# Kernel optimization log

Hardware: AMD Instinct MI355X
Metric: run time of the kernel (lower is better)

Reference implementation:

```python
import jax, jax.numpy as jnp
import numpy as np

N_QUBITS = 4
N_LAYERS = 2
MARGIN = 0.3
BATCH = 524288
DIM = 2 ** N_QUBITS  # 16


def _apply_ry(state, theta, q):
    # state: [B, 16] complex; theta: [B] real; RY on qubit q (qubit 0 = MSB)
    B = state.shape[0]
    lead = 2 ** q
    rest = 2 ** (N_QUBITS - q - 1)
    s = state.reshape(B, lead, 2, rest)
    c = jnp.cos(theta * 0.5)[:, None, None]
    sn = jnp.sin(theta * 0.5)[:, None, None]
    a0, a1 = s[:, :, 0, :], s[:, :, 1, :]
    out = jnp.stack([c * a0 - sn * a1, sn * a0 + c * a1], axis=2)
    return out.reshape(B, DIM)


def _apply_rz(state, theta, q):
    B = state.shape[0]
    lead = 2 ** q
    rest = 2 ** (N_QUBITS - q - 1)
    s = state.reshape(B, lead, 2, rest)
    ph = jnp.exp(1j * (theta * 0.5)).astype(jnp.complex64)[:, None, None]
    a0, a1 = s[:, :, 0, :], s[:, :, 1, :]
    out = jnp.stack([jnp.conj(ph) * a0, ph * a1], axis=2)
    return out.reshape(B, DIM)


def _apply_cnot(state, c, t):
    # c < t; control qubit c, target qubit t
    B = state.shape[0]
    s = state.reshape((B,) + (2,) * N_QUBITS)
    s0 = jnp.take(s, 0, axis=c + 1)
    s1 = jnp.take(s, 1, axis=c + 1)
    s1 = jnp.flip(s1, axis=t)  # t > c: target axis shifts to t after removing axis c+1
    out = jnp.stack([s0, s1], axis=c + 1)
    return out.reshape(B, DIM)


def _simulate(ry, rz):
    # ry, rz: [B, N_LAYERS, N_QUBITS] -> statevector [B, 16] complex64
    B = ry.shape[0]
    state = jnp.zeros((B, DIM), dtype=jnp.complex64).at[:, 0].set(1.0)
    for l in range(N_LAYERS):
        for q in range(N_QUBITS):
            state = _apply_ry(state, ry[:, l, q], q)
            state = _apply_rz(state, rz[:, l, q], q)
        for q in range(N_QUBITS - 1):  # linear entangling chain
            state = _apply_cnot(state, q, q + 1)
    return state


def setup_inputs() -> dict:
    key = jax.random.key(0)
    ks = jax.random.split(key, 6)
    shape = (BATCH, N_LAYERS, N_QUBITS)
    names = ["anchor_ry", "anchor_rz", "positive_ry", "positive_rz",
             "negative_ry", "negative_rz"]
    return {n: jax.random.normal(k, shape, dtype=jnp.float32)
            for n, k in zip(names, ks)}


def reference(anchor_ry, anchor_rz, positive_ry, positive_rz,
              negative_ry, negative_rz):
    psi_a = _simulate(anchor_ry, anchor_rz)
    psi_p = _simulate(positive_ry, positive_rz)
    psi_n = _simulate(negative_ry, negative_rz)
    # fidelity |<a|b>|^2 per sample
    ov_p = jnp.sum(jnp.conj(psi_a) * psi_p, axis=-1)
    ov_n = jnp.sum(jnp.conj(psi_a) * psi_n, axis=-1)
    fid_pos = jnp.abs(ov_p) ** 2
    fid_neg = jnp.abs(ov_n) ** 2
    loss = jnp.maximum(MARGIN - fid_pos + fid_neg, 0.0)
    return loss.mean()
```

## Files before the change

### kernel.cpp

```cpp
#include <hip/hip_runtime.h>

typedef float v2f __attribute__((ext_vector_type(2)));

constexpr int NQ = 4;
constexpr int DIM = 16;
constexpr float MARGIN = 0.3f;
constexpr float INV2PI = 0.15915494309189535f;

__device__ __forceinline__ v2f mk2(float x, float y) { v2f r; r.x = x; r.y = y; return r; }

__device__ __forceinline__ v2f cmul_pre(v2f a, v2f b, v2f bs) {
  return a.xx * b + a.yy * bs;
}

__device__ __forceinline__ void sincos_hw(float rev, float& s, float& c) {
  s = __builtin_amdgcn_sinf(rev);
  c = __builtin_amdgcn_cosf(rev);
}

__device__ __forceinline__ void cnot_ladder(v2f s[DIM]) {
#pragma unroll
  for (int q = 0; q < NQ - 1; ++q) {
    const int pc = 1 << (NQ - 1 - q);
    const int pt = 1 << (NQ - 2 - q);
#pragma unroll
    for (int i = 0; i < DIM; ++i) {
      if ((i & pc) && !(i & pt)) {
        const int j = i | pt;
        v2f t = s[i]; s[i] = s[j]; s[j] = t;
      }
    }
  }
}

__device__ __forceinline__ void simulate(const float ry[8], const float rz[8], v2f s[DIM]) {
  float c0[NQ]; v2f p1[NQ], p1s[NQ];
#pragma unroll
  for (int q = 0; q < NQ; ++q) {
    float sy, cy; sincos_hw(ry[q] * (0.5f * INV2PI), sy, cy);
    float sz, cz; sincos_hw(rz[q] * INV2PI, sz, cz);
    c0[q]  = cy;
    p1[q]  = mk2(sy * cz, sy * sz);
    p1s[q] = mk2(-p1[q].y, p1[q].x);
  }
  v2f t2[4];
  t2[0] = mk2(c0[0] * c0[1], 0.0f);
  t2[1] = c0[0] * p1[1];
  t2[2] = c0[1] * p1[0];
  t2[3] = cmul_pre(p1[0], p1[1], p1s[1]);
  v2f t3[8];
#pragma unroll
  for (int k = 0; k < 4; ++k) {
    t3[2*k]   = t2[k] * c0[2];
    t3[2*k+1] = cmul_pre(t2[k], p1[2], p1s[2]);
  }
#pragma unroll
  for (int k = 0; k < 8; ++k) {
    s[2*k]   = t3[k] * c0[3];
    s[2*k+1] = cmul_pre(t3[k], p1[3], p1s[3]);
  }

  cnot_ladder(s);

#pragma unroll
  for (int q = 0; q < NQ; ++q) {
    const int bit = 1 << (NQ - 1 - q);
    float sy, cy; sincos_hw(ry[4 + q] * (0.5f * INV2PI), sy, cy);
#pragma unroll
    for (int i = 0; i < DIM; ++i) {
      if (i & bit) continue;
      const int j = i | bit;
      const v2f a0 = s[i], a1 = s[j];
      s[i] = cy * a0 - sy * a1;
      s[j] = sy * a0 + cy * a1;
    }
    float sz, cz; sincos_hw(rz[4 + q] * INV2PI, sz, cz);
    const v2f ph  = mk2(cz, sz);
    const v2f phs = mk2(-sz, cz);
#pragma unroll
    for (int i = 0; i < DIM; ++i) {
      if (i & bit) s[i] = cmul_pre(s[i], ph, phs);
    }
  }
}

__device__ __forceinline__ float fidelity(const v2f a[DIM], const v2f x[DIM]) {
  v2f ov1 = mk2(0.f, 0.f), ov2 = mk2(0.f, 0.f);
#pragma unroll
  for (int i = 0; i < DIM; ++i) {
    ov1 += a[i].xx * x[i];
    ov2 += a[i].yy * x[i].yx;
  }
  const float ovr = ov1.x + ov2.x;
  const float ovi = ov1.y - ov2.y;
  return ovr * ovr + ovi * ovi;
}

__device__ __forceinline__ void load8(const float* __restrict__ p, int b, float a[8]) {
  const float4* v = reinterpret_cast<const float4*>(p) + (size_t)b * 2;
  float4 x0 = v[0], x1 = v[1];
  a[0]=x0.x; a[1]=x0.y; a[2]=x0.z; a[3]=x0.w;
  a[4]=x1.x; a[5]=x1.y; a[6]=x1.z; a[7]=x1.w;
}

__global__ __launch_bounds__(256) void triplet_main(
    const float* __restrict__ a_ry, const float* __restrict__ a_rz,
    const float* __restrict__ p_ry, const float* __restrict__ p_rz,
    const float* __restrict__ n_ry, const float* __restrict__ n_rz,
    float* __restrict__ block_sums, int batch) {
  const int b = blockIdx.x * blockDim.x + threadIdx.x;

  float loss = 0.0f;
  if (b < batch) {
    float ry[8], rz[8];
    load8(a_ry, b, ry); load8(a_rz, b, rz);
    v2f as[DIM];
    simulate(ry, rz, as);

    load8(p_ry, b, ry); load8(p_rz, b, rz);
    v2f xs[DIM];
    simulate(ry, rz, xs);
    const float fid_pos = fidelity(as, xs);

    load8(n_ry, b, ry); load8(n_rz, b, rz);
    simulate(ry, rz, xs);
    const float fid_neg = fidelity(as, xs);

    loss = fmaxf(MARGIN - fid_pos + fid_neg, 0.0f);
  }

#pragma unroll
  for (int off = 32; off >= 1; off >>= 1)
    loss += __shfl_down(loss, off, 64);

  __shared__ float wsum[4];
  const int lane = threadIdx.x & 63;
  const int wid  = threadIdx.x >> 6;
  if (lane == 0) wsum[wid] = loss;
  __syncthreads();
  if (threadIdx.x == 0) {
    block_sums[blockIdx.x] = wsum[0] + wsum[1] + wsum[2] + wsum[3];
  }
}

__global__ __launch_bounds__(256) void triplet_reduce(
    const float* __restrict__ block_sums, int nblocks, float* __restrict__ out, float inv_batch) {
  float s = 0.0f;
  for (int i = threadIdx.x; i < nblocks; i += 256) s += block_sums[i];
#pragma unroll
  for (int off = 32; off >= 1; off >>= 1)
    s += __shfl_down(s, off, 64);

  __shared__ float wsum[4];
  const int lane = threadIdx.x & 63;
  const int wid  = threadIdx.x >> 6;
  if (lane == 0) wsum[wid] = s;
  __syncthreads();
  if (threadIdx.x == 0) {
    out[0] = (wsum[0] + wsum[1] + wsum[2] + wsum[3]) * inv_batch;
  }
}

extern "C" void kernel_launch(void* const* d_in, const int* in_sizes, int n_in,
                              void* d_out, int out_size, void* d_ws, size_t ws_size,
                              hipStream_t stream) {
  const float* a_ry = (const float*)d_in[0];
  const float* a_rz = (const float*)d_in[1];
  const float* p_ry = (const float*)d_in[2];
  const float* p_rz = (const float*)d_in[3];
  const float* n_ry = (const float*)d_in[4];
  const float* n_rz = (const float*)d_in[5];
  float* out = (float*)d_out;

  const int batch = in_sizes[0] / 8;
  const int nblocks = (batch + 255) / 256;
  float* block_sums = (float*)d_ws;

  triplet_main<<<nblocks, 256, 0, stream>>>(a_ry, a_rz, p_ry, p_rz, n_ry, n_rz,
                                            block_sums, batch);
  triplet_reduce<<<1, 256, 0, stream>>>(block_sums, nblocks, out, 1.0f / (float)batch);
}
```

Baseline: 29.46 us.

## Fold anchor's final RZ phases into other states and fuse reduction via last-block atomic

Drops the last-layer RZ from the anchor state and applies only the phase differences (rz_p - rz_a, rz_n - rz_a) to the positive and negative states. This works because the overlap's magnitude is unchanged by the common diagonal phase. It also interleaves the positive and negative simulations for ILP and loads all inputs up front. The separate reduce kernel is replaced by a last-block-done atomic counter, at the cost of a memset launch and threadfences.

```diff
diff --git a/kernel.cpp b/kernel.cpp
--- a/kernel.cpp
+++ b/kernel.cpp
@@ -33,7 +33,7 @@
   }
 }
 
-__device__ __forceinline__ void simulate(const float ry[8], const float rz[8], v2f s[DIM]) {
+__device__ __forceinline__ void layer1_cl(const float ry[8], const float rz[8], v2f s[DIM]) {
   float c0[NQ]; v2f p1[NQ], p1s[NQ];
 #pragma unroll
   for (int q = 0; q < NQ; ++q) {
@@ -59,9 +59,10 @@
     s[2*k]   = t3[k] * c0[3];
     s[2*k+1] = cmul_pre(t3[k], p1[3], p1s[3]);
   }
-
   cnot_ladder(s);
-
+}
+
+__device__ __forceinline__ void ry_layer(const float ry[8], v2f s[DIM]) {
 #pragma unroll
   for (int q = 0; q < NQ; ++q) {
     const int bit = 1 << (NQ - 1 - q);
@@ -74,26 +75,7 @@
       s[i] = cy * a0 - sy * a1;
       s[j] = sy * a0 + cy * a1;
     }
-    float sz, cz; sincos_hw(rz[4 + q] * INV2PI, sz, cz);
-    const v2f ph  = mk2(cz, sz);
-    const v2f phs = mk2(-sz, cz);
-#pragma unroll
-    for (int i = 0; i < DIM; ++i) {
-      if (i & bit) s[i] = cmul_pre(s[i], ph, phs);
-    }
-  }
-}
-
-__device__ __forceinline__ float fidelity(const v2f a[DIM], const v2f x[DIM]) {
-  v2f ov1 = mk2(0.f, 0.f), ov2 = mk2(0.f, 0.f);
-#pragma unroll
-  for (int i = 0; i < DIM; ++i) {
-    ov1 += a[i].xx * x[i];
-    ov2 += a[i].yy * x[i].yx;
-  }
-  const float ovr = ov1.x + ov2.x;
-  const float ovi = ov1.y - ov2.y;
-  return ovr * ovr + ovi * ovi;
+  }
 }
 
 __device__ __forceinline__ void load8(const float* __restrict__ p, int b, float a[8]) {
@@ -103,28 +85,77 @@
   a[4]=x1.x; a[5]=x1.y; a[6]=x1.z; a[7]=x1.w;
 }
 
-__global__ __launch_bounds__(256) void triplet_main(
+__global__ __launch_bounds__(256) void triplet_fused(
     const float* __restrict__ a_ry, const float* __restrict__ a_rz,
     const float* __restrict__ p_ry, const float* __restrict__ p_rz,
     const float* __restrict__ n_ry, const float* __restrict__ n_rz,
-    float* __restrict__ block_sums, int batch) {
+    float* __restrict__ partials, unsigned* __restrict__ counter,
+    float* __restrict__ out, int batch) {
   const int b = blockIdx.x * blockDim.x + threadIdx.x;
 
   float loss = 0.0f;
   if (b < batch) {
-    float ry[8], rz[8];
-    load8(a_ry, b, ry); load8(a_rz, b, rz);
+    float ary[8], arz[8];
+    load8(a_ry, b, ary); load8(a_rz, b, arz);
     v2f as[DIM];
-    simulate(ry, rz, as);
-
-    load8(p_ry, b, ry); load8(p_rz, b, rz);
-    v2f xs[DIM];
-    simulate(ry, rz, xs);
-    const float fid_pos = fidelity(as, xs);
-
-    load8(n_ry, b, ry); load8(n_rz, b, rz);
-    simulate(ry, rz, xs);
-    const float fid_neg = fidelity(as, xs);
+    layer1_cl(ary, arz, as);
+    ry_layer(ary, as);
+
+    float pry[8], prz[8], nry[8], nrz[8];
+    load8(p_ry, b, pry); load8(p_rz, b, prz);
+    load8(n_ry, b, nry); load8(n_rz, b, nrz);
+
+    v2f xs[DIM], ys[DIM];
+    layer1_cl(pry, prz, xs);
+    layer1_cl(nry, nrz, ys);
+
+#pragma unroll
+    for (int q = 0; q < NQ; ++q) {
+      const int bit = 1 << (NQ - 1 - q);
+      float syp, cyp; sincos_hw(pry[4 + q] * (0.5f * INV2PI), syp, cyp);
+      float syn, cyn; sincos_hw(nry[4 + q] * (0.5f * INV2PI), syn, cyn);
+#pragma unroll
+      for (int i = 0; i < DIM; ++i) {
+        if (i & bit) continue;
+        const int j = i | bit;
+        const v2f x0 = xs[i], x1 = xs[j];
+        xs[i] = cyp * x0 - syp * x1;
+        xs[j] = syp * x0 + cyp * x1;
+        const v2f y0 = ys[i], y1 = ys[j];
+        ys[i] = cyn * y0 - syn * y1;
+        ys[j] = syn * y0 + cyn * y1;
+      }
+    }
+
+#pragma unroll
+    for (int q = 0; q < NQ; ++q) {
+      const int bit = 1 << (NQ - 1 - q);
+      float szp, czp; sincos_hw((prz[4 + q] - arz[4 + q]) * INV2PI, szp, czp);
+      float szn, czn; sincos_hw((nrz[4 + q] - arz[4 + q]) * INV2PI, szn, czn);
+      const v2f php  = mk2(czp, szp), phps = mk2(-szp, czp);
+      const v2f phn  = mk2(czn, szn), phns = mk2(-szn, czn);
+#pragma unroll
+      for (int i = 0; i < DIM; ++i) {
+        if (i & bit) {
+          xs[i] = cmul_pre(xs[i], php, phps);
+          ys[i] = cmul_pre(ys[i], phn, phns);
+        }
+      }
+    }
+
+    v2f op1 = mk2(0.f,0.f), op2 = mk2(0.f,0.f);
+    v2f on1 = mk2(0.f,0.f), on2 = mk2(0.f,0.f);
+#pragma unroll
+    for (int i = 0; i < DIM; ++i) {
+      op1 += as[i].xx * xs[i];
+      op2 += as[i].yy * xs[i].yx;
+      on1 += as[i].xx * ys[i];
+      on2 += as[i].yy * ys[i].yx;
+    }
+    const float opr = op1.x + op2.x, opi = op1.y - op2.y;
+    const float onr = on1.x + on2.x, oni = on1.y - on2.y;
+    const float fid_pos = opr*opr + opi*opi;
+    const float fid_neg = onr*onr + oni*oni;
 
     loss = fmaxf(MARGIN - fid_pos + fid_neg, 0.0f);
   }
@@ -138,26 +169,27 @@
   const int wid  = threadIdx.x >> 6;
   if (lane == 0) wsum[wid] = loss;
   __syncthreads();
+
+  __shared__ bool amLast;
   if (threadIdx.x == 0) {
-    block_sums[blockIdx.x] = wsum[0] + wsum[1] + wsum[2] + wsum[3];
-  }
-}
-
-__global__ __launch_bounds__(256) void triplet_reduce(
-    const float* __restrict__ block_sums, int nblocks, float* __restrict__ out, float inv_batch) {
-  float s = 0.0f;
-  for (int i = threadIdx.x; i < nblocks; i += 256) s += block_sums[i];
-#pragma unroll
-  for (int off = 32; off >= 1; off >>= 1)
-    s += __shfl_down(s, off, 64);
-
-  __shared__ float wsum[4];
-  const int lane = threadIdx.x & 63;
-  const int wid  = threadIdx.x >> 6;
-  if (lane == 0) wsum[wid] = s;
+    partials[blockIdx.x] = wsum[0] + wsum[1] + wsum[2] + wsum[3];
+    __threadfence();
+    unsigned old = atomicAdd(counter, 1u);
+    amLast = (old == gridDim.x - 1);
+  }
   __syncthreads();
-  if (threadIdx.x == 0) {
-    out[0] = (wsum[0] + wsum[1] + wsum[2] + wsum[3]) * inv_batch;
+
+  if (amLast) {
+    __threadfence();
+    float s = 0.0f;
+    for (int i = threadIdx.x; i < (int)gridDim.x; i += 256) s += partials[i];
+#pragma unroll
+    for (int off = 32; off >= 1; off >>= 1)
+      s += __shfl_down(s, off, 64);
+    if (lane == 0) wsum[wid] = s;
+    __syncthreads();
+    if (threadIdx.x == 0)
+      out[0] = (wsum[0] + wsum[1] + wsum[2] + wsum[3]) / (float)batch;
   }
 }
 
@@ -174,9 +206,12 @@
 
   const int batch = in_sizes[0] / 8;
   const int nblocks = (batch + 255) / 256;
-  float* block_sums = (float*)d_ws;
-
-  triplet_main<<<nblocks, 256, 0, stream>>>(a_ry, a_rz, p_ry, p_rz, n_ry, n_rz,
-                                            block_sums, batch);
-  triplet_reduce<<<1, 256, 0, stream>>>(block_sums, nblocks, out, 1.0f / (float)batch);
-}
+
+  float* partials = (float*)d_ws;
+  unsigned* counter = (unsigned*)((char*)d_ws + (size_t)nblocks * sizeof(float));
+
+  hipMemsetAsync(counter, 0, sizeof(unsigned), stream);
+
+  triplet_fused<<<nblocks, 256, 0, stream>>>(a_ry, a_rz, p_ry, p_rz, n_ry, n_rz,
+                                             partials, counter, out, batch);
+}
```

New measurement: 86.91 us. 2.95x slower.

## Fold final RZ layer into relative phase and fuse reduction via last-block atomic

Applied to the files above, without the earlier changes.

The last-layer RZ gates are diagonal, so the overlap only depends on the difference of the final RZ angles. Instead of applying them to every state, only the positive and negative states get a phase of the angle difference, which drops the anchor's final RZ sincos and multiplies. The separate reduce kernel is replaced by a last-block-done pattern: an atomic counter plus threadfence, with the final block summing the partials. This adds a memset launch and an atomic per block, and sets launch_bounds min blocks to 1.

```diff
diff --git a/kernel.cpp b/kernel.cpp
--- a/kernel.cpp
+++ b/kernel.cpp
@@ -33,7 +33,7 @@
   }
 }
 
-__device__ __forceinline__ void simulate(const float ry[8], const float rz[8], v2f s[DIM]) {
+__device__ __forceinline__ void sim_core(const float ry[8], const float rz[8], v2f s[DIM]) {
   float c0[NQ]; v2f p1[NQ], p1s[NQ];
 #pragma unroll
   for (int q = 0; q < NQ; ++q) {
@@ -74,17 +74,21 @@
       s[i] = cy * a0 - sy * a1;
       s[j] = sy * a0 + cy * a1;
     }
-    float sz, cz; sincos_hw(rz[4 + q] * INV2PI, sz, cz);
+  }
+}
+
+__device__ __forceinline__ float fid_with_dz(const v2f a[DIM], v2f x[DIM], const float dz[NQ]) {
+#pragma unroll
+  for (int q = 0; q < NQ; ++q) {
+    const int bit = 1 << (NQ - 1 - q);
+    float sz, cz; sincos_hw(dz[q] * INV2PI, sz, cz);
     const v2f ph  = mk2(cz, sz);
     const v2f phs = mk2(-sz, cz);
 #pragma unroll
     for (int i = 0; i < DIM; ++i) {
-      if (i & bit) s[i] = cmul_pre(s[i], ph, phs);
+      if (i & bit) x[i] = cmul_pre(x[i], ph, phs);
     }
   }
-}
-
-__device__ __forceinline__ float fidelity(const v2f a[DIM], const v2f x[DIM]) {
   v2f ov1 = mk2(0.f, 0.f), ov2 = mk2(0.f, 0.f);
 #pragma unroll
   for (int i = 0; i < DIM; ++i) {
@@ -103,28 +107,37 @@
   a[4]=x1.x; a[5]=x1.y; a[6]=x1.z; a[7]=x1.w;
 }
 
-__global__ __launch_bounds__(256) void triplet_main(
+__global__ __launch_bounds__(256, 1) void triplet_fused(
     const float* __restrict__ a_ry, const float* __restrict__ a_rz,
     const float* __restrict__ p_ry, const float* __restrict__ p_rz,
     const float* __restrict__ n_ry, const float* __restrict__ n_rz,
-    float* __restrict__ block_sums, int batch) {
+    float* __restrict__ partials, unsigned* __restrict__ counter,
+    float* __restrict__ out, int batch) {
   const int b = blockIdx.x * blockDim.x + threadIdx.x;
 
   float loss = 0.0f;
   if (b < batch) {
-    float ry[8], rz[8];
+    float ry[8], rz[8], arz2[NQ];
+
     load8(a_ry, b, ry); load8(a_rz, b, rz);
+#pragma unroll
+    for (int q = 0; q < NQ; ++q) arz2[q] = rz[4 + q];
     v2f as[DIM];
-    simulate(ry, rz, as);
+    sim_core(ry, rz, as);
 
     load8(p_ry, b, ry); load8(p_rz, b, rz);
     v2f xs[DIM];
-    simulate(ry, rz, xs);
-    const float fid_pos = fidelity(as, xs);
+    sim_core(ry, rz, xs);
+    float dz[NQ];
+#pragma unroll
+    for (int q = 0; q < NQ; ++q) dz[q] = rz[4 + q] - arz2[q];
+    const float fid_pos = fid_with_dz(as, xs, dz);
 
     load8(n_ry, b, ry); load8(n_rz, b, rz);
-    simulate(ry, rz, xs);
-    const float fid_neg = fidelity(as, xs);
+    sim_core(ry, rz, xs);
+#pragma unroll
+    for (int q = 0; q < NQ; ++q) dz[q] = rz[4 + q] - arz2[q];
+    const float fid_neg = fid_with_dz(as, xs, dz);
 
     loss = fmaxf(MARGIN - fid_pos + fid_neg, 0.0f);
   }
@@ -138,26 +151,27 @@
   const int wid  = threadIdx.x >> 6;
   if (lane == 0) wsum[wid] = loss;
   __syncthreads();
+
+  __shared__ bool amLast;
   if (threadIdx.x == 0) {
-    block_sums[blockIdx.x] = wsum[0] + wsum[1] + wsum[2] + wsum[3];
+    partials[blockIdx.x] = wsum[0] + wsum[1] + wsum[2] + wsum[3];
+    __threadfence();
+    unsigned old = atomicAdd(counter, 1u);
+    amLast = (old == gridDim.x - 1);
   }
-}
+  __syncthreads();
 
-__global__ __launch_bounds__(256) void triplet_reduce(
-    const float* __restrict__ block_sums, int nblocks, float* __restrict__ out, float inv_batch) {
-  float s = 0.0f;
-  for (int i = threadIdx.x; i < nblocks; i += 256) s += block_sums[i];
+  if (amLast) {
+    __threadfence();
+    float s = 0.0f;
+    for (int i = threadIdx.x; i < (int)gridDim.x; i += 256) s += partials[i];
 #pragma unroll
-  for (int off = 32; off >= 1; off >>= 1)
-    s += __shfl_down(s, off, 64);
-
-  __shared__ float wsum[4];
-  const int lane = threadIdx.x & 63;
-  const int wid  = threadIdx.x >> 6;
-  if (lane == 0) wsum[wid] = s;
-  __syncthreads();
-  if (threadIdx.x == 0) {
-    out[0] = (wsum[0] + wsum[1] + wsum[2] + wsum[3]) * inv_batch;
+    for (int off = 32; off >= 1; off >>= 1)
+      s += __shfl_down(s, off, 64);
+    if (lane == 0) wsum[wid] = s;
+    __syncthreads();
+    if (threadIdx.x == 0)
+      out[0] = (wsum[0] + wsum[1] + wsum[2] + wsum[3]) / (float)batch;
   }
 }
 
@@ -174,9 +188,12 @@
 
   const int batch = in_sizes[0] / 8;
   const int nblocks = (batch + 255) / 256;
-  float* block_sums = (float*)d_ws;
 
-  triplet_main<<<nblocks, 256, 0, stream>>>(a_ry, a_rz, p_ry, p_rz, n_ry, n_rz,
-                                            block_sums, batch);
-  triplet_reduce<<<1, 256, 0, stream>>>(block_sums, nblocks, out, 1.0f / (float)batch);
+  float* partials = (float*)d_ws;
+  unsigned* counter = (unsigned*)((char*)d_ws + (size_t)nblocks * sizeof(float));
+
+  hipMemsetAsync(counter, 0, sizeof(unsigned), stream);
+
+  triplet_fused<<<nblocks, 256, 0, stream>>>(a_ry, a_rz, p_ry, p_rz, n_ry, n_rz,
+                                             partials, counter, out, batch);
 }
```

Result: slower. 87.07 us (+195.6%).

## Fold final RZ layer into relative phase and use SoA packed statevector

Applied to the files above, without the earlier changes.

Restructures the per-sample simulation into split real/imaginary arrays packed as float2 pairs, so packed FMA ops apply. The CNOT ladder is removed by permuting the basis indices through a table. The last-layer RZ rotations are dropped from each state and applied once as the difference of angles on the partner state inside the fidelity, since the anchor's diagonal phases cancel in the overlap magnitude. This cuts transcendental and complex-multiply work per triplet, but relies on that algebraic identity and a careful reindexing.

```diff
diff --git a/kernel.cpp b/kernel.cpp
--- a/kernel.cpp
+++ b/kernel.cpp
@@ -2,98 +2,115 @@
 
 typedef float v2f __attribute__((ext_vector_type(2)));
 
-constexpr int NQ = 4;
-constexpr int DIM = 16;
 constexpr float MARGIN = 0.3f;
 constexpr float INV2PI = 0.15915494309189535f;
 
 __device__ __forceinline__ v2f mk2(float x, float y) { v2f r; r.x = x; r.y = y; return r; }
-
-__device__ __forceinline__ v2f cmul_pre(v2f a, v2f b, v2f bs) {
-  return a.xx * b + a.yy * bs;
-}
 
 __device__ __forceinline__ void sincos_hw(float rev, float& s, float& c) {
   s = __builtin_amdgcn_sinf(rev);
   c = __builtin_amdgcn_cosf(rev);
 }
 
-__device__ __forceinline__ void cnot_ladder(v2f s[DIM]) {
-#pragma unroll
-  for (int q = 0; q < NQ - 1; ++q) {
-    const int pc = 1 << (NQ - 1 - q);
-    const int pt = 1 << (NQ - 2 - q);
-#pragma unroll
-    for (int i = 0; i < DIM; ++i) {
-      if ((i & pc) && !(i & pt)) {
-        const int j = i | pt;
-        v2f t = s[i]; s[i] = s[j]; s[j] = t;
-      }
-    }
-  }
-}
-
-__device__ __forceinline__ void simulate(const float ry[8], const float rz[8], v2f s[DIM]) {
-  float c0[NQ]; v2f p1[NQ], p1s[NQ];
-#pragma unroll
-  for (int q = 0; q < NQ; ++q) {
+__device__ __forceinline__ void sim_core(const float ry[8], const float rz[8],
+                                         v2f R[8], v2f I[8]) {
+  float c0[4], p1r[4], p1i[4];
+#pragma unroll
+  for (int q = 0; q < 4; ++q) {
     float sy, cy; sincos_hw(ry[q] * (0.5f * INV2PI), sy, cy);
     float sz, cz; sincos_hw(rz[q] * INV2PI, sz, cz);
-    c0[q]  = cy;
-    p1[q]  = mk2(sy * cz, sy * sz);
-    p1s[q] = mk2(-p1[q].y, p1[q].x);
-  }
-  v2f t2[4];
-  t2[0] = mk2(c0[0] * c0[1], 0.0f);
-  t2[1] = c0[0] * p1[1];
-  t2[2] = c0[1] * p1[0];
-  t2[3] = cmul_pre(p1[0], p1[1], p1s[1]);
-  v2f t3[8];
+    c0[q] = cy; p1r[q] = sy * cz; p1i[q] = sy * sz;
+  }
+  float t2r[4], t2i[4];
+  t2r[0] = c0[0]*c0[1];                     t2i[0] = 0.0f;
+  t2r[1] = c0[0]*p1r[1];                    t2i[1] = c0[0]*p1i[1];
+  t2r[2] = p1r[0]*c0[1];                    t2i[2] = p1i[0]*c0[1];
+  t2r[3] = p1r[0]*p1r[1] - p1i[0]*p1i[1];   t2i[3] = p1r[0]*p1i[1] + p1i[0]*p1r[1];
+  float t3r[8], t3i[8];
 #pragma unroll
   for (int k = 0; k < 4; ++k) {
-    t3[2*k]   = t2[k] * c0[2];
-    t3[2*k+1] = cmul_pre(t2[k], p1[2], p1s[2]);
-  }
-#pragma unroll
-  for (int k = 0; k < 8; ++k) {
-    s[2*k]   = t3[k] * c0[3];
-    s[2*k+1] = cmul_pre(t3[k], p1[3], p1s[3]);
-  }
-
-  cnot_ladder(s);
-
-#pragma unroll
-  for (int q = 0; q < NQ; ++q) {
-    const int bit = 1 << (NQ - 1 - q);
-    float sy, cy; sincos_hw(ry[4 + q] * (0.5f * INV2PI), sy, cy);
-#pragma unroll
-    for (int i = 0; i < DIM; ++i) {
-      if (i & bit) continue;
-      const int j = i | bit;
-      const v2f a0 = s[i], a1 = s[j];
-      s[i] = cy * a0 - sy * a1;
-      s[j] = sy * a0 + cy * a1;
-    }
-    float sz, cz; sincos_hw(rz[4 + q] * INV2PI, sz, cz);
-    const v2f ph  = mk2(cz, sz);
-    const v2f phs = mk2(-sz, cz);
-#pragma unroll
-    for (int i = 0; i < DIM; ++i) {
-      if (i & bit) s[i] = cmul_pre(s[i], ph, phs);
-    }
-  }
-}
-
-__device__ __forceinline__ float fidelity(const v2f a[DIM], const v2f x[DIM]) {
-  v2f ov1 = mk2(0.f, 0.f), ov2 = mk2(0.f, 0.f);
-#pragma unroll
-  for (int i = 0; i < DIM; ++i) {
-    ov1 += a[i].xx * x[i];
-    ov2 += a[i].yy * x[i].yx;
-  }
-  const float ovr = ov1.x + ov2.x;
-  const float ovi = ov1.y - ov2.y;
-  return ovr * ovr + ovi * ovi;
+    t3r[2*k]   = t2r[k]*c0[2];                  t3i[2*k]   = t2i[k]*c0[2];
+    t3r[2*k+1] = t2r[k]*p1r[2] - t2i[k]*p1i[2]; t3i[2*k+1] = t2r[k]*p1i[2] + t2i[k]*p1r[2];
+  }
+  constexpr int tab[8] = {0, 1, 3, 2, 6, 7, 5, 4};
+  const float c3 = c0[3], qr = p1r[3], qi = p1i[3];
+#pragma unroll
+  for (int w = 0; w < 8; ++w) {
+    const int k = tab[w];
+    const float e0r = t3r[k]*c3,             e0i = t3i[k]*c3;
+    const float e1r = t3r[k]*qr - t3i[k]*qi, e1i = t3r[k]*qi + t3i[k]*qr;
+    if (w & 1) { R[w] = mk2(e1r, e0r); I[w] = mk2(e1i, e0i); }
+    else       { R[w] = mk2(e0r, e1r); I[w] = mk2(e0i, e1i); }
+  }
+
+  float sy[4], cy[4];
+#pragma unroll
+  for (int q = 0; q < 4; ++q) sincos_hw(ry[4+q] * (0.5f * INV2PI), sy[q], cy[q]);
+#pragma unroll
+  for (int w = 0; w < 4; ++w) {
+    const v2f r0 = R[w], r1 = R[w+4], i0 = I[w], i1 = I[w+4];
+    R[w]   = cy[0]*r0 - sy[0]*r1;  R[w+4] = sy[0]*r0 + cy[0]*r1;
+    I[w]   = cy[0]*i0 - sy[0]*i1;  I[w+4] = sy[0]*i0 + cy[0]*i1;
+  }
+#pragma unroll
+  for (int m = 0; m < 4; ++m) {
+    const int w = (m & 1) | ((m & 2) << 1);
+    const v2f r0 = R[w], r1 = R[w+2], i0 = I[w], i1 = I[w+2];
+    R[w]   = cy[1]*r0 - sy[1]*r1;  R[w+2] = sy[1]*r0 + cy[1]*r1;
+    I[w]   = cy[1]*i0 - sy[1]*i1;  I[w+2] = sy[1]*i0 + cy[1]*i1;
+  }
+#pragma unroll
+  for (int m = 0; m < 4; ++m) {
+    const int w = 2*m;
+    const v2f r0 = R[w], r1 = R[w+1], i0 = I[w], i1 = I[w+1];
+    R[w]   = cy[2]*r0 - sy[2]*r1;  R[w+1] = sy[2]*r0 + cy[2]*r1;
+    I[w]   = cy[2]*i0 - sy[2]*i1;  I[w+1] = sy[2]*i0 + cy[2]*i1;
+  }
+#pragma unroll
+  for (int w = 0; w < 8; ++w) {
+    const v2f r = R[w], i = I[w];
+    R[w] = cy[3]*r + sy[3]*mk2(-r.y, r.x);
+    I[w] = cy[3]*i + sy[3]*mk2(-i.y, i.x);
+  }
+}
+
+__device__ __forceinline__ float fid_soa(const v2f AR[8], const v2f AI[8],
+                                         v2f XR[8], v2f XI[8], const float dz[4]) {
+  float sz[4], cz[4];
+#pragma unroll
+  for (int q = 0; q < 4; ++q) sincos_hw(dz[q] * INV2PI, sz[q], cz[q]);
+#pragma unroll
+  for (int w = 4; w < 8; ++w) {
+    const v2f r = XR[w], i = XI[w];
+    XR[w] = cz[0]*r - sz[0]*i;  XI[w] = sz[0]*r + cz[0]*i;
+  }
+#pragma unroll
+  for (int m = 0; m < 4; ++m) {
+    const int w = (m & 1) | 2 | ((m & 2) << 1);
+    const v2f r = XR[w], i = XI[w];
+    XR[w] = cz[1]*r - sz[1]*i;  XI[w] = sz[1]*r + cz[1]*i;
+  }
+#pragma unroll
+  for (int m = 0; m < 4; ++m) {
+    const int w = 2*m + 1;
+    const v2f r = XR[w], i = XI[w];
+    XR[w] = cz[2]*r - sz[2]*i;  XI[w] = sz[2]*r + cz[2]*i;
+  }
+  const v2f Cv = mk2(1.0f, cz[3]), Sv = mk2(0.0f, sz[3]);
+#pragma unroll
+  for (int w = 0; w < 8; ++w) {
+    const v2f r = XR[w], i = XI[w];
+    XR[w] = r*Cv - i*Sv;  XI[w] = i*Cv + r*Sv;
+  }
+  v2f s1 = mk2(0.f, 0.f), s2 = mk2(0.f, 0.f);
+#pragma unroll
+  for (int w = 0; w < 8; ++w) {
+    s1 += AR[w]*XR[w];  s1 += AI[w]*XI[w];
+    s2 += AR[w]*XI[w];  s2 -= AI[w]*XR[w];
+  }
+  const float ovr = s1.x + s1.y;
+  const float ovi = s2.x + s2.y;
+  return ovr*ovr + ovi*ovi;
 }
 
 __device__ __forceinline__ void load8(const float* __restrict__ p, int b, float a[8]) {
@@ -112,19 +129,27 @@
 
   float loss = 0.0f;
   if (b < batch) {
-    float ry[8], rz[8];
+    float ry[8], rz[8], arz2[4];
+
     load8(a_ry, b, ry); load8(a_rz, b, rz);
-    v2f as[DIM];
-    simulate(ry, rz, as);
+#pragma unroll
+    for (int q = 0; q < 4; ++q) arz2[q] = rz[4 + q];
+    v2f AR[8], AI[8];
+    sim_core(ry, rz, AR, AI);
 
     load8(p_ry, b, ry); load8(p_rz, b, rz);
-    v2f xs[DIM];
-    simulate(ry, rz, xs);
-    const float fid_pos = fidelity(as, xs);
+    v2f XR[8], XI[8];
+    sim_core(ry, rz, XR, XI);
+    float dz[4];
+#pragma unroll
+    for (int q = 0; q < 4; ++q) dz[q] = rz[4 + q] - arz2[q];
+    const float fid_pos = fid_soa(AR, AI, XR, XI, dz);
 
     load8(n_ry, b, ry); load8(n_rz, b, rz);
-    simulate(ry, rz, xs);
-    const float fid_neg = fidelity(as, xs);
+    sim_core(ry, rz, XR, XI);
+#pragma unroll
+    for (int q = 0; q < 4; ++q) dz[q] = rz[4 + q] - arz2[q];
+    const float fid_neg = fid_soa(AR, AI, XR, XI, dz);
 
     loss = fmaxf(MARGIN - fid_pos + fid_neg, 0.0f);
   }
```

Result: slower. 31.42 us (+6.7%).
